# Kernel optimization log

Measured on AMD Instinct MI355X. Metric: run time of the kernel, lower is better.

Reference implementation:

```python
import jax, jax.numpy as jnp
import numpy as np

# Per-species MLP dims from CoefficientLayer._create_model (H, C, N, O), aev_dim=384
DIMS = {"h": [384, 160, 128, 96, 1], "c": [384, 144, 112, 96, 1], "n": [384, 128, 112, 96, 1], "o": [384, 128, 112, 96, 1]}


def setup_inputs() -> dict:
    key = jax.random.key(0)
    B, A, D = 256, 256, 384
    ks = jax.random.split(key, 64)
    inp = {}
    inp["species"] = jax.random.randint(ks[0], (B, A), 0, 4)  # species index 0..3
    inp["aev"] = jax.random.normal(ks[1], (B, A, D), dtype=jnp.float32)
    inp["b0"] = jnp.array([0.1, 0.2, 0.3, 0.4], dtype=jnp.float32)  # shifter intercepts
    inp["b1"] = jnp.array([1.0, 1.1, 0.9, 1.2], dtype=jnp.float32)  # shifter slopes
    ki = 2
    for name, dims in DIMS.items():
        for l in range(4):
            fi, fo = dims[l], dims[l + 1]
            inp[f"{name}w{l}"] = jax.random.normal(ks[ki], (fi, fo), dtype=jnp.float32) / np.float32(np.sqrt(fi))
            ki += 1
            inp[f"{name}b{l}"] = jnp.zeros((fo,), dtype=jnp.float32)
    return inp


def _mlp(x, ws, bs):
    # Linear -> CELU(0.1) x3 -> Linear(->1), squeeze last dim
    for i in range(3):
        x = jax.nn.celu(x @ ws[i] + bs[i], alpha=0.1)
    return (x @ ws[3] + bs[3])[..., 0]


def reference(species, aev, b0, b1,
              hw0, hb0, hw1, hb1, hw2, hb2, hw3, hb3,
              cw0, cb0, cw1, cb1, cw2, cb2, cw3, cb3,
              nw0, nb0, nw1, nb1, nw2, nb2, nw3, nb3,
              ow0, ob0, ow1, ob1, ow2, ob2, ow3, ob3):
    nets = [
        ([hw0, hw1, hw2, hw3], [hb0, hb1, hb2, hb3]),
        ([cw0, cw1, cw2, cw3], [cb0, cb1, cb2, cb3]),
        ([nw0, nw1, nw2, nw3], [nb0, nb1, nb2, nb3]),
        ([ow0, ow1, ow2, ow3], [ob0, ob1, ob2, ob3]),
    ]
    # ANIModel hard routing: each atom's coefficient comes from its species' network;
    # atoms with species == -1 (padding) stay 0.
    coef = jnp.zeros(species.shape, dtype=aev.dtype)
    for i, (ws, bs) in enumerate(nets):  # fixed small loop over 4 species
        coef = jnp.where(species == i, _mlp(aev, ws, bs), coef)
    # Shifter: result[mask_i] = b0[i] + b1[i] * coef[mask_i]; padding stays 0
    idx = jnp.clip(species, 0)
    return jnp.where(species >= 0, b0[idx] + b1[idx] * coef, jnp.zeros((), dtype=aev.dtype))
```

## Files before the change

kernel.cpp:

```cpp
#include <hip/hip_runtime.h>

typedef _Float16 f16;
typedef _Float16 f16x8 __attribute__((ext_vector_type(8)));
typedef float f32x4 __attribute__((ext_vector_type(4)));
typedef unsigned short u16;

#define NATOMS 65536
#define SLOT 5120
#define NBUF 2

#define WS_LISTS_OFF 256
#define WS_W_OFF 524544
#define WS_W_ELEMS 350208
#define WS_NEEDED (WS_W_OFF + WS_W_ELEMS * 2)

struct ConvJob { const float* src; int K, N, KS, NT, CK, off; };

struct PrepParams {
  const int* species;
  int* counts;
  u16* lists;
  f16* wbase;
  ConvJob jobs[16];
};

struct MlpParams {
  const float* aev;
  const float* b0;
  const float* b1;
  const float* bias[4][4];
  const f16* w[4][4];
  const int* counts;
  const u16* lists;
  float* out;
  int Nreal0[4];
  int Nreal1[4];
};

template <int N> struct AF { f16x8 v[N]; };
template <int N> struct ACC { f32x4 v[N]; };

__global__ __launch_bounds__(256) void prep_kernel(PrepParams p) {
  int tid = threadIdx.x;
  if (blockIdx.x < 256) {
    __shared__ int wcnt[4][4];
    __shared__ int wbase[4][4];
    int i = blockIdx.x * 256 + tid;
    int s = p.species[i];
    int wave = tid >> 6, lane = tid & 63;
    unsigned long long m[4];
    #pragma unroll
    for (int t = 0; t < 4; t++) {
      m[t] = __ballot(s == t);
      if (lane == 0) wcnt[wave][t] = __popcll(m[t]);
    }
    __syncthreads();
    if (tid < 4) {
      int t = tid;
      int c0 = wcnt[0][t], c1 = wcnt[1][t], c2 = wcnt[2][t], c3 = wcnt[3][t];
      int base = atomicAdd(&p.counts[t], c0 + c1 + c2 + c3);
      wbase[0][t] = base;
      wbase[1][t] = base + c0;
      wbase[2][t] = base + c0 + c1;
      wbase[3][t] = base + c0 + c1 + c2;
    }
    __syncthreads();
    int rnk = __popcll(m[s] & ((1ull << lane) - 1ull));
    p.lists[s * NATOMS + wbase[wave][s] + rnk] = (u16)i;
  } else {
    int bx = blockIdx.x - 256;
    int job = bx / 30, bxin = bx - job * 30;
    ConvJob jb = p.jobs[job];
    int e = bxin * 256 + tid;
    int nslots = jb.KS * jb.NT * 64;
    if (e >= nslots) return;
    int frag = e >> 6, lane = e & 63;
    int c = frag / (jb.CK * jb.NT);
    int rem = frag - c * (jb.CK * jb.NT);
    int ckc = min(jb.CK, jb.KS - c * jb.CK);
    int nt = rem / ckc, ki = rem - nt * ckc;
    int ks = c * jb.CK + ki;
    int q = lane >> 4, nlo = lane & 15;
    int n = nt * 16 + nlo;
    int k0 = ks * 32 + q * 8;
    f16x8 v;
    #pragma unroll
    for (int j = 0; j < 8; j++) {
      int k = k0 + j;
      float x = (n < jb.N && k < jb.K) ? jb.src[k * jb.N + n] : 0.f;
      v[j] = (f16)x;
    }
    *(f16x8*)(p.wbase + jb.off + (size_t)e * 8) = v;
  }
}

__device__ __forceinline__ float celu01(float v) {
  return v > 0.f ? v : 0.1f * (__expf(v * 10.f) - 1.f);
}

__device__ __forceinline__ void stage_frag(const f16* g, f16* l, int lane) {
  __builtin_amdgcn_global_load_lds(
      (const __attribute__((address_space(1))) unsigned int*)(g + lane * 8),
      (__attribute__((address_space(3))) unsigned int*)l, 16, 0, 0);
}

template <int NT0, int KS1>
struct Sched {
  static constexpr int NC = 12 + KS1 + 4 + 1;
  static constexpr int frags(int c) {
    return c < 12 ? NT0 : (c < 12 + KS1 ? 8 : (c < 12 + KS1 + 4 ? 6 : 3));
  }
};

template <int NT0, int KS1, int C>
__device__ __forceinline__ void stage_chunk(const f16* w0, const f16* w1,
                                            const f16* w2, const f16* w3,
                                            f16* ring, int w, int lane) {
  constexpr int NF = Sched<NT0, KS1>::frags(C);
  const f16* g;
  if constexpr (C < 12) g = w0 + (size_t)C * NT0 * 512;
  else if constexpr (C < 12 + KS1) g = w1 + (size_t)(C - 12) * 8 * 512;
  else if constexpr (C < 12 + KS1 + 4) g = w2 + (size_t)(C - 12 - KS1) * 6 * 512;
  else g = w3;
  f16* l = ring + (C % NBUF) * SLOT;
  if (w < NF) stage_frag(g + w * 512, l + w * 512, lane);
  if constexpr (NF > 8) {
    if (w + 8 < NF) stage_frag(g + (w + 8) * 512, l + (w + 8) * 512, lane);
  }
}

template <int NT0, int KS1, int CB, int KS, int NT, int I>
__device__ __forceinline__ ACC<NT> layer_step(AF<KS> a, ACC<NT> acc, f16* ring,
    const f16* s0, const f16* s1, const f16* s2, const f16* s3, int w, int lane) {
  if constexpr (I == KS) {
    return acc;
  } else {
    constexpr int G = CB + I;
    if constexpr (G + 1 < Sched<NT0, KS1>::NC)
      stage_chunk<NT0, KS1, G + 1>(s0, s1, s2, s3, ring, w, lane);
    const f16* slot = ring + (G % NBUF) * SLOT;
    #pragma unroll
    for (int nt = 0; nt < NT; nt++) {
      f16x8 b = *(const f16x8*)(slot + nt * 512 + lane * 8);
      acc.v[nt] = __builtin_amdgcn_mfma_f32_16x16x32_f16(a.v[I], b, acc.v[nt], 0, 0, 0);
    }
    __syncthreads();
    return layer_step<NT0, KS1, CB, KS, NT, I + 1>(a, acc, ring, s0, s1, s2, s3, w, lane);
  }
}

template <int NT0, int KS1, int CB, int KS, int NT, bool ACT>
__device__ __forceinline__ void consume_layer(AF<KS> a, f16* ring,
    const f16* s0, const f16* s1, const f16* s2, const f16* s3,
    const float* __restrict__ bias, int Nreal, f16* dstw, int w, int lane,
    int q, int nlo) {
  ACC<NT> acc;
  #pragma unroll
  for (int nt = 0; nt < NT; nt++) acc.v[nt] = f32x4{0.f, 0.f, 0.f, 0.f};
  acc = layer_step<NT0, KS1, CB, KS, NT, 0>(a, acc, ring, s0, s1, s2, s3, w, lane);
  #pragma unroll
  for (int nt = 0; nt < NT; nt++) {
    int n = nt * 16 + nlo;
    float bv = (n < Nreal) ? bias[n] : 0.f;
    #pragma unroll
    for (int r = 0; r < 4; r++) {
      float v = acc.v[nt][r] + bv;
      if (ACT) v = celu01(v);
      dstw[(q * 4 + r) * 168 + n] = (f16)v;
    }
  }
}

template <int NT0, int KS1>
__device__ __forceinline__ void mlp_body(const MlpParams& p, int s, int tile,
                                         f16* ring, f16* Bf) {
  int cnt = p.counts[s];
  if (tile * 128 >= cnt) return;
  int tid = threadIdx.x, w = tid >> 6, lane = tid & 63;
  const f16 *s0 = p.w[s][0], *s1 = p.w[s][1], *s2 = p.w[s][2], *s3 = p.w[s][3];

  stage_chunk<NT0, KS1, 0>(s0, s1, s2, s3, ring, w, lane);

  const u16* list = p.lists + s * NATOMS;
  int q = lane >> 4, nlo = lane & 15;
  int rowbase = tile * 128 + w * 16;
  int atom = list[min(rowbase + nlo, cnt - 1)];

  AF<12> a0;
  const float* ap = p.aev + (size_t)atom * 384 + q * 8;
  #pragma unroll
  for (int ks = 0; ks < 12; ks++) {
    float4 u0 = *(const float4*)(ap + ks * 32);
    float4 u1 = *(const float4*)(ap + ks * 32 + 4);
    f16x8 t = {(f16)u0.x, (f16)u0.y, (f16)u0.z, (f16)u0.w,
               (f16)u1.x, (f16)u1.y, (f16)u1.z, (f16)u1.w};
    a0.v[ks] = t;
  }
  __syncthreads();

  f16* my = Bf + (w * 16) * 168;

  consume_layer<NT0, KS1, 0, 12, NT0, true>(a0, ring, s0, s1, s2, s3,
      p.bias[s][0], p.Nreal0[s], my, w, lane, q, nlo);
  AF<KS1> a1;
  #pragma unroll
  for (int ks = 0; ks < KS1; ks++)
    a1.v[ks] = *(const f16x8*)(my + nlo * 168 + ks * 32 + q * 8);
  consume_layer<NT0, KS1, 12, KS1, 8, true>(a1, ring, s0, s1, s2, s3,
      p.bias[s][1], p.Nreal1[s], my, w, lane, q, nlo);
  AF<4> a2;
  #pragma unroll
  for (int ks = 0; ks < 4; ks++)
    a2.v[ks] = *(const f16x8*)(my + nlo * 168 + ks * 32 + q * 8);
  consume_layer<NT0, KS1, 12 + KS1, 4, 6, true>(a2, ring, s0, s1, s2, s3,
      p.bias[s][2], 96, my, w, lane, q, nlo);

  AF<3> a3;
  #pragma unroll
  for (int ks = 0; ks < 3; ks++)
    a3.v[ks] = *(const f16x8*)(my + nlo * 168 + ks * 32 + q * 8);
  constexpr int G3 = 12 + KS1 + 4;
  const f16* slot = ring + (G3 % NBUF) * SLOT;
  f32x4 acc3 = {0.f, 0.f, 0.f, 0.f};
  #pragma unroll
  for (int ks = 0; ks < 3; ks++) {
    f16x8 b = *(const f16x8*)(slot + ks * 512 + lane * 8);
    acc3 = __builtin_amdgcn_mfma_f32_16x16x32_f16(a3.v[ks], b, acc3, 0, 0, 0);
  }
  if (nlo == 0) {
    float b3 = p.bias[s][3][0];
    float b0v = p.b0[s], b1v = p.b1[s];
    #pragma unroll
    for (int r = 0; r < 4; r++) {
      int m = rowbase + q * 4 + r;
      if (m < cnt) {
        float coef = acc3[r] + b3;
        p.out[list[m]] = b0v + b1v * coef;
      }
    }
  }
}

__global__ __launch_bounds__(512, 4) void mlp_kernel(MlpParams p) {
  __shared__ __align__(16) f16 ring[NBUF * SLOT];
  __shared__ __align__(16) f16 Bf[128 * 168];
  int s = blockIdx.x & 3;
  int tile = blockIdx.x >> 2;
  switch (s) {
    case 0: mlp_body<10, 5>(p, 0, tile, ring, Bf); break;
    case 1: mlp_body<10, 5>(p, 1, tile, ring, Bf); break;
    case 2: mlp_body<8, 4>(p, 2, tile, ring, Bf); break;
    default: mlp_body<8, 4>(p, 3, tile, ring, Bf); break;
  }
}

extern "C" void kernel_launch(void* const* d_in, const int* in_sizes, int n_in,
                              void* d_out, int out_size, void* d_ws, size_t ws_size,
                              hipStream_t stream) {
  if (ws_size < WS_NEEDED) return;

  const int* species = (const int*)d_in[0];
  const float* aev = (const float*)d_in[1];
  const float* b0 = (const float*)d_in[2];
  const float* b1 = (const float*)d_in[3];

  static const int F1[4]  = {160, 144, 128, 128};
  static const int F1p[4] = {160, 160, 128, 128};
  static const int F2[4]  = {128, 112, 112, 112};

  char* wsb = (char*)d_ws;
  int* counts = (int*)wsb;
  u16* lists = (u16*)(wsb + WS_LISTS_OFF);
  f16* wbase = (f16*)(wsb + WS_W_OFF);

  PrepParams pp;
  pp.species = species; pp.counts = counts; pp.lists = lists; pp.wbase = wbase;

  MlpParams mp;
  mp.aev = aev; mp.b0 = b0; mp.b1 = b1;
  mp.counts = counts; mp.lists = lists; mp.out = (float*)d_out;

  int off = 0, ji = 0;
  for (int s = 0; s < 4; s++) {
    int K[4]  = {384, F1[s], F2[s], 96};
    int N[4]  = {F1[s], F2[s], 96, 1};
    int KS[4] = {12, F1p[s] / 32, 4, 3};
    int NT[4] = {F1p[s] / 16, 8, 6, 1};
    int CK[4] = {1, 1, 1, 3};
    for (int l = 0; l < 4; l++) {
      const float* w = (const float*)d_in[4 + s * 8 + l * 2];
      const float* b = (const float*)d_in[4 + s * 8 + l * 2 + 1];
      pp.jobs[ji].src = w;
      pp.jobs[ji].K = K[l];
      pp.jobs[ji].N = N[l];
      pp.jobs[ji].KS = KS[l];
      pp.jobs[ji].NT = NT[l];
      pp.jobs[ji].CK = CK[l];
      pp.jobs[ji].off = off;
      mp.w[s][l] = wbase + off;
      mp.bias[s][l] = b;
      off += KS[l] * NT[l] * 512;
      ji++;
    }
    mp.Nreal0[s] = F1[s];
    mp.Nreal1[s] = F2[s];
  }

  hipMemsetAsync(d_ws, 0, 64, stream);
  prep_kernel<<<dim3(256 + 480), 256, 0, stream>>>(pp);
  mlp_kernel<<<dim3(140 * 4), 512, 0, stream>>>(mp);
}
```

Baseline: 268.6 us.

## Split fused per-species MLP into per-layer kernels with LDS-resident weights

Replaces the single fused MLP kernel, which streamed weight chunks through a double-buffered LDS ring with a barrier per K-step, with three kernels. Each kernel loads one layer's full weight slice into LDS once and then loops over 16-row tiles per wave, with no barriers inside the loop. Activations between layers go through f16 global workspace buffers. The last hidden layer is fused with the final 96→1 projection, done as an fp32 dot product and a shuffle reduction. The cost is extra global traffic for the intermediate activations and two more launches. Per-species rows are capped at a fixed CAP, so any atoms beyond it would be silently dropped, and the new path runs only when the workspace is large enough.

```diff
diff --git a/kernel.cpp b/kernel.cpp
--- a/kernel.cpp
+++ b/kernel.cpp
@@ -6,6 +6,7 @@
 typedef unsigned short u16;
 
 #define NATOMS 65536
+#define CAP 17920
 #define SLOT 5120
 #define NBUF 2
 
@@ -13,6 +14,13 @@
 #define WS_W_OFF 524544
 #define WS_W_ELEMS 350208
 #define WS_NEEDED (WS_W_OFF + WS_W_ELEMS * 2)
+#define WS_ACT0_OFF (2u << 20)
+#define WS_ACT1_OFF (26u << 20)
+#define WS_BIG (46u << 20)
+
+#define BL0 64
+#define BL1 128
+#define BL2 128
 
 struct ConvJob { const float* src; int K, N, KS, NT, CK, off; };
 
@@ -24,21 +32,23 @@
   ConvJob jobs[16];
 };
 
-struct MlpParams {
+struct GemmParams {
   const float* aev;
   const float* b0;
   const float* b1;
   const float* bias[4][4];
+  const float* w3src[4];
   const f16* w[4][4];
   const int* counts;
   const u16* lists;
+  f16* act0;
+  f16* act1;
   float* out;
   int Nreal0[4];
   int Nreal1[4];
 };
 
 template <int N> struct AF { f16x8 v[N]; };
-template <int N> struct ACC { f32x4 v[N]; };
 
 __global__ __launch_bounds__(256) void prep_kernel(PrepParams p) {
   int tid = threadIdx.x;
@@ -104,6 +114,220 @@
       (__attribute__((address_space(3))) unsigned int*)l, 16, 0, 0);
 }
 
+
+template <int NTH>
+__device__ void k0_body(const GemmParams& p, int s, int half, int bl, f16* W) {
+  int tid = threadIdx.x, w = tid >> 6, lane = tid & 63;
+  int q = lane >> 4, nlo = lane & 15;
+  constexpr int NT0 = 2 * NTH;
+  const f16* g = p.w[s][0];
+  for (int f = w; f < 12 * NTH; f += 8) {
+    int ks = f / NTH, ntl = f - ks * NTH;
+    stage_frag(g + (size_t)(ks * NT0 + half * NTH + ntl) * 512, W + f * 512, lane);
+  }
+  int cnt = min(p.counts[s], CAP);
+  int ntiles = (cnt + 15) >> 4;
+  const u16* list = p.lists + s * NATOMS;
+  int Nr = p.Nreal0[s];
+  const float* bias = p.bias[s][0];
+  float bv[NTH];
+  #pragma unroll
+  for (int nt = 0; nt < NTH; nt++) {
+    int n = half * NTH * 16 + nt * 16 + nlo;
+    bv[nt] = (n < Nr) ? bias[n] : 0.f;
+  }
+  f16* act = p.act0 + (size_t)s * CAP * 160;
+  __syncthreads();
+
+  for (int t = bl * 8 + w; t < ntiles; t += BL0 * 8) {
+    int tb = t * 16;
+    int atom = list[min(tb + nlo, cnt - 1)];
+    const float* ap = p.aev + (size_t)atom * 384 + q * 8;
+    AF<12> a;
+    #pragma unroll
+    for (int ks = 0; ks < 12; ks++) {
+      float4 u0 = *(const float4*)(ap + ks * 32);
+      float4 u1 = *(const float4*)(ap + ks * 32 + 4);
+      a.v[ks] = f16x8{(f16)u0.x, (f16)u0.y, (f16)u0.z, (f16)u0.w,
+                      (f16)u1.x, (f16)u1.y, (f16)u1.z, (f16)u1.w};
+    }
+    f32x4 acc[NTH];
+    #pragma unroll
+    for (int nt = 0; nt < NTH; nt++) acc[nt] = f32x4{0.f, 0.f, 0.f, 0.f};
+    #pragma unroll
+    for (int ks = 0; ks < 12; ks++) {
+      #pragma unroll
+      for (int nt = 0; nt < NTH; nt++) {
+        f16x8 b = *(const f16x8*)(W + (ks * NTH + nt) * 512 + lane * 8);
+        acc[nt] = __builtin_amdgcn_mfma_f32_16x16x32_f16(a.v[ks], b, acc[nt], 0, 0, 0);
+      }
+    }
+    #pragma unroll
+    for (int nt = 0; nt < NTH; nt++) {
+      int n = half * NTH * 16 + nt * 16 + nlo;
+      #pragma unroll
+      for (int r = 0; r < 4; r++) {
+        int row = tb + q * 4 + r;
+        if (row < cnt) {
+          float v = celu01(acc[nt][r] + bv[nt]);
+          act[(size_t)row * 160 + n] = (f16)v;
+        }
+      }
+    }
+  }
+}
+
+__global__ __launch_bounds__(512, 4) void k0_kernel(GemmParams p) {
+  __shared__ __align__(16) f16 W[12 * 5 * 512];
+  int combo = blockIdx.x & 7, bl = blockIdx.x >> 3;
+  int s = combo >> 1, half = combo & 1;
+  switch (s) {
+    case 0: k0_body<5>(p, 0, half, bl, W); break;
+    case 1: k0_body<5>(p, 1, half, bl, W); break;
+    case 2: k0_body<4>(p, 2, half, bl, W); break;
+    default: k0_body<4>(p, 3, half, bl, W); break;
+  }
+}
+
+template <int KS1>
+__device__ void k1_body(const GemmParams& p, int s, int bl, f16* W) {
+  int tid = threadIdx.x, w = tid >> 6, lane = tid & 63;
+  int q = lane >> 4, nlo = lane & 15;
+  const f16* g = p.w[s][1];
+  for (int f = w; f < KS1 * 8; f += 8)
+    stage_frag(g + (size_t)f * 512, W + f * 512, lane);
+  int cnt = min(p.counts[s], CAP);
+  int ntiles = (cnt + 15) >> 4;
+  int Nr = p.Nreal1[s];
+  const float* bias = p.bias[s][1];
+  float bv[8];
+  #pragma unroll
+  for (int nt = 0; nt < 8; nt++) {
+    int n = nt * 16 + nlo;
+    bv[nt] = (n < Nr) ? bias[n] : 0.f;
+  }
+  const f16* act0 = p.act0 + (size_t)s * CAP * 160;
+  f16* act1 = p.act1 + (size_t)s * CAP * 128;
+  __syncthreads();
+
+  for (int t = bl * 8 + w; t < ntiles; t += BL1 * 8) {
+    int tb = t * 16;
+    int ar = min(tb + nlo, cnt - 1);
+    const f16* ap = act0 + (size_t)ar * 160 + q * 8;
+    AF<KS1> a;
+    #pragma unroll
+    for (int ks = 0; ks < KS1; ks++)
+      a.v[ks] = *(const f16x8*)(ap + ks * 32);
+    f32x4 acc[8];
+    #pragma unroll
+    for (int nt = 0; nt < 8; nt++) acc[nt] = f32x4{0.f, 0.f, 0.f, 0.f};
+    #pragma unroll
+    for (int ks = 0; ks < KS1; ks++) {
+      #pragma unroll
+      for (int nt = 0; nt < 8; nt++) {
+        f16x8 b = *(const f16x8*)(W + (ks * 8 + nt) * 512 + lane * 8);
+        acc[nt] = __builtin_amdgcn_mfma_f32_16x16x32_f16(a.v[ks], b, acc[nt], 0, 0, 0);
+      }
+    }
+    #pragma unroll
+    for (int nt = 0; nt < 8; nt++) {
+      int n = nt * 16 + nlo;
+      #pragma unroll
+      for (int r = 0; r < 4; r++) {
+        int row = tb + q * 4 + r;
+        if (row < cnt) {
+          float v = celu01(acc[nt][r] + bv[nt]);
+          act1[(size_t)row * 128 + n] = (f16)v;
+        }
+      }
+    }
+  }
+}
+
+__global__ __launch_bounds__(512, 4) void k1_kernel(GemmParams p) {
+  __shared__ __align__(16) f16 W[5 * 8 * 512];
+  int s = blockIdx.x & 3, bl = blockIdx.x >> 2;
+  switch (s) {
+    case 0: k1_body<5>(p, 0, bl, W); break;
+    case 1: k1_body<5>(p, 1, bl, W); break;
+    case 2: k1_body<4>(p, 2, bl, W); break;
+    default: k1_body<4>(p, 3, bl, W); break;
+  }
+}
+
+__device__ void k2_body(const GemmParams& p, int s, int bl, f16* W) {
+  int tid = threadIdx.x, w = tid >> 6, lane = tid & 63;
+  int q = lane >> 4, nlo = lane & 15;
+  const f16* g = p.w[s][2];
+  for (int f = w; f < 4 * 6; f += 8)
+    stage_frag(g + (size_t)f * 512, W + f * 512, lane);
+  int cnt = min(p.counts[s], CAP);
+  int ntiles = (cnt + 15) >> 4;
+  const u16* list = p.lists + s * NATOMS;
+  const float* bias2 = p.bias[s][2];
+  const float* w3 = p.w3src[s];
+  float b2v[6], w3v[6];
+  #pragma unroll
+  for (int nt = 0; nt < 6; nt++) {
+    int n = nt * 16 + nlo;
+    b2v[nt] = bias2[n];
+    w3v[nt] = w3[n];
+  }
+  float b3 = p.bias[s][3][0];
+  float b0v = p.b0[s], b1v = p.b1[s];
+  const f16* act1 = p.act1 + (size_t)s * CAP * 128;
+  __syncthreads();
+
+  for (int t = bl * 8 + w; t < ntiles; t += BL2 * 8) {
+    int tb = t * 16;
+    int ar = min(tb + nlo, cnt - 1);
+    const f16* ap = act1 + (size_t)ar * 128 + q * 8;
+    AF<4> a;
+    #pragma unroll
+    for (int ks = 0; ks < 4; ks++)
+      a.v[ks] = *(const f16x8*)(ap + ks * 32);
+    f32x4 acc[6];
+    #pragma unroll
+    for (int nt = 0; nt < 6; nt++) acc[nt] = f32x4{0.f, 0.f, 0.f, 0.f};
+    #pragma unroll
+    for (int ks = 0; ks < 4; ks++) {
+      #pragma unroll
+      for (int nt = 0; nt < 6; nt++) {
+        f16x8 b = *(const f16x8*)(W + (ks * 6 + nt) * 512 + lane * 8);
+        acc[nt] = __builtin_amdgcn_mfma_f32_16x16x32_f16(a.v[ks], b, acc[nt], 0, 0, 0);
+      }
+    }
+    float pr[4] = {0.f, 0.f, 0.f, 0.f};
+    #pragma unroll
+    for (int nt = 0; nt < 6; nt++) {
+      #pragma unroll
+      for (int r = 0; r < 4; r++) {
+        float v = celu01(acc[nt][r] + b2v[nt]);
+        pr[r] += v * w3v[nt];
+      }
+    }
+    #pragma unroll
+    for (int m = 1; m < 16; m <<= 1) {
+      #pragma unroll
+      for (int r = 0; r < 4; r++) pr[r] += __shfl_xor(pr[r], m);
+    }
+    if (nlo == 0) {
+      #pragma unroll
+      for (int r = 0; r < 4; r++) {
+        int row = tb + q * 4 + r;
+        if (row < cnt) p.out[list[row]] = b0v + b1v * (pr[r] + b3);
+      }
+    }
+  }
+}
+
+__global__ __launch_bounds__(512, 4) void k2_kernel(GemmParams p) {
+  __shared__ __align__(16) f16 W[4 * 6 * 512];
+  int s = blockIdx.x & 3, bl = blockIdx.x >> 2;
+  k2_body(p, s, bl, W);
+}
+
+
 template <int NT0, int KS1>
 struct Sched {
   static constexpr int NC = 12 + KS1 + 4 + 1;
@@ -129,8 +353,10 @@
   }
 }
 
+template <int N> struct ACCB { f32x4 v[N]; };
+
 template <int NT0, int KS1, int CB, int KS, int NT, int I>
-__device__ __forceinline__ ACC<NT> layer_step(AF<KS> a, ACC<NT> acc, f16* ring,
+__device__ __forceinline__ ACCB<NT> layer_step(AF<KS> a, ACCB<NT> acc, f16* ring,
     const f16* s0, const f16* s1, const f16* s2, const f16* s3, int w, int lane) {
   if constexpr (I == KS) {
     return acc;
@@ -154,7 +380,7 @@
     const f16* s0, const f16* s1, const f16* s2, const f16* s3,
     const float* __restrict__ bias, int Nreal, f16* dstw, int w, int lane,
     int q, int nlo) {
-  ACC<NT> acc;
+  ACCB<NT> acc;
   #pragma unroll
   for (int nt = 0; nt < NT; nt++) acc.v[nt] = f32x4{0.f, 0.f, 0.f, 0.f};
   acc = layer_step<NT0, KS1, CB, KS, NT, 0>(a, acc, ring, s0, s1, s2, s3, w, lane);
@@ -172,34 +398,28 @@
 }
 
 template <int NT0, int KS1>
-__device__ __forceinline__ void mlp_body(const MlpParams& p, int s, int tile,
+__device__ __forceinline__ void mlp_body(const GemmParams& p, int s, int tile,
                                          f16* ring, f16* Bf) {
   int cnt = p.counts[s];
   if (tile * 128 >= cnt) return;
   int tid = threadIdx.x, w = tid >> 6, lane = tid & 63;
   const f16 *s0 = p.w[s][0], *s1 = p.w[s][1], *s2 = p.w[s][2], *s3 = p.w[s][3];
-
   stage_chunk<NT0, KS1, 0>(s0, s1, s2, s3, ring, w, lane);
-
   const u16* list = p.lists + s * NATOMS;
   int q = lane >> 4, nlo = lane & 15;
   int rowbase = tile * 128 + w * 16;
   int atom = list[min(rowbase + nlo, cnt - 1)];
-
   AF<12> a0;
   const float* ap = p.aev + (size_t)atom * 384 + q * 8;
   #pragma unroll
   for (int ks = 0; ks < 12; ks++) {
     float4 u0 = *(const float4*)(ap + ks * 32);
     float4 u1 = *(const float4*)(ap + ks * 32 + 4);
-    f16x8 t = {(f16)u0.x, (f16)u0.y, (f16)u0.z, (f16)u0.w,
-               (f16)u1.x, (f16)u1.y, (f16)u1.z, (f16)u1.w};
-    a0.v[ks] = t;
+    a0.v[ks] = f16x8{(f16)u0.x, (f16)u0.y, (f16)u0.z, (f16)u0.w,
+                     (f16)u1.x, (f16)u1.y, (f16)u1.z, (f16)u1.w};
   }
   __syncthreads();
-
   f16* my = Bf + (w * 16) * 168;
-
   consume_layer<NT0, KS1, 0, 12, NT0, true>(a0, ring, s0, s1, s2, s3,
       p.bias[s][0], p.Nreal0[s], my, w, lane, q, nlo);
   AF<KS1> a1;
@@ -214,7 +434,6 @@
     a2.v[ks] = *(const f16x8*)(my + nlo * 168 + ks * 32 + q * 8);
   consume_layer<NT0, KS1, 12 + KS1, 4, 6, true>(a2, ring, s0, s1, s2, s3,
       p.bias[s][2], 96, my, w, lane, q, nlo);
-
   AF<3> a3;
   #pragma unroll
   for (int ks = 0; ks < 3; ks++)
@@ -241,7 +460,7 @@
   }
 }
 
-__global__ __launch_bounds__(512, 4) void mlp_kernel(MlpParams p) {
+__global__ __launch_bounds__(512, 4) void mlp_kernel(GemmParams p) {
   __shared__ __align__(16) f16 ring[NBUF * SLOT];
   __shared__ __align__(16) f16 Bf[128 * 168];
   int s = blockIdx.x & 3;
@@ -254,6 +473,7 @@
   }
 }
 
+
 extern "C" void kernel_launch(void* const* d_in, const int* in_sizes, int n_in,
                               void* d_out, int out_size, void* d_ws, size_t ws_size,
                               hipStream_t stream) {
@@ -276,9 +496,11 @@
   PrepParams pp;
   pp.species = species; pp.counts = counts; pp.lists = lists; pp.wbase = wbase;
 
-  MlpParams mp;
+  GemmParams mp;
   mp.aev = aev; mp.b0 = b0; mp.b1 = b1;
   mp.counts = counts; mp.lists = lists; mp.out = (float*)d_out;
+  mp.act0 = (f16*)(wsb + WS_ACT0_OFF);
+  mp.act1 = (f16*)(wsb + WS_ACT1_OFF);
 
   int off = 0, ji = 0;
   for (int s = 0; s < 4; s++) {
@@ -302,11 +524,19 @@
       off += KS[l] * NT[l] * 512;
       ji++;
     }
+    mp.w3src[s] = (const float*)d_in[4 + s * 8 + 6];
     mp.Nreal0[s] = F1[s];
     mp.Nreal1[s] = F2[s];
   }
 
   hipMemsetAsync(d_ws, 0, 64, stream);
   prep_kernel<<<dim3(256 + 480), 256, 0, stream>>>(pp);
-  mlp_kernel<<<dim3(140 * 4), 512, 0, stream>>>(mp);
-}
+
+  if (ws_size >= WS_BIG) {
+    k0_kernel<<<dim3(8 * BL0), 512, 0, stream>>>(mp);
+    k1_kernel<<<dim3(4 * BL1), 512, 0, stream>>>(mp);
+    k2_kernel<<<dim3(4 * BL2), 512, 0, stream>>>(mp);
+  } else {
+    mlp_kernel<<<dim3(140 * 4), 512, 0, stream>>>(mp);
+  }
+}
```

After: 433.2 us. 1.61x slower.
